# Kernel optimization log

Measured on AMD Instinct MI355X. Metric: run time of the kernel, lower is better.

The kernel has to match this reference:

```python
import jax, jax.numpy as jnp
import numpy as np

NUM_HEADS = 8
TOPK = 16


def setup_inputs() -> dict:
    key = jax.random.key(0)
    ks = jax.random.split(key, 13)
    B, C, H, W = 2, 512, 64, 64
    Hu, Wu = H // 2, W // 2
    hd = C // NUM_HEADS
    n = lambda k, shape, s=1.0: jax.random.normal(k, shape, dtype=jnp.float32) * s
    return {
        "x": n(ks[0], (B, C, H, W)),
        "upper_feat": n(ks[1], (B, C, Hu, Wu)),
        "gumbel": jax.random.gumbel(ks[2], (B, NUM_HEADS, Hu * Wu), dtype=jnp.float32),
        # 1x1 convs (Conv2d + folded eval-mode BN => weight matrix + bias)
        "q_w": n(ks[3], (C, C), 0.02), "q_b": n(ks[4], (C,), 0.02),
        "kv_w": n(ks[5], (2 * C, C), 0.02), "kv_b": n(ks[6], (2 * C,), 0.02),
        "proj_w": n(ks[7], (C, C), 0.02), "proj_b": n(ks[8], (C,), 0.02),
        # depthwise 7x7 PE conv (groups = C)
        "pe_w": n(ks[9], (C, 1, 7, 7), 0.02), "pe_b": n(ks[10], (C,), 0.02),
        # gate conv1d kernel_size=1: [head_dim, 2*head_dim]
        "gate_w": n(ks[11], (hd, 2 * hd), 0.02), "gate_b": n(ks[12], (hd,), 0.02),
    }


def reference(x, upper_feat, gumbel, q_w, q_b, kv_w, kv_b, proj_w, proj_b,
              pe_w, pe_b, gate_w, gate_b):
    B, C, H, W = x.shape
    hd = C // NUM_HEADS
    Hu, Wu = upper_feat.shape[2], upper_feat.shape[3]
    N, Nu = H * W, Hu * Wu
    scale = hd ** -0.5

    def conv1x1(t, w, b):
        return jnp.einsum('bchw,oc->bohw', t, w) + b[None, :, None, None]

    # coarse attention: q from x, k/v from upper_feat
    q = conv1x1(x, q_w, q_b).reshape(B, NUM_HEADS, hd, N).transpose(0, 1, 3, 2)          # [B,h,N,d]
    kv = conv1x1(upper_feat, kv_w, kv_b).reshape(B, NUM_HEADS, 2 * hd, Nu).transpose(0, 1, 3, 2)
    k, v = kv[..., :hd], kv[..., hd:]                                                    # [B,h,Nu,d]
    sim = jnp.einsum('bhnd,bhmd->bhnm', q, k) * scale                                    # [B,h,N,Nu]
    attn = jax.nn.softmax(sim, axis=-1)
    coarse = jnp.einsum('bhnm,bhmd->bhnd', attn, v)                                      # [B,h,N,d]

    # fine branch: kv from x, top-k token selection via gumbel-softmax scores
    f_kv = conv1x1(x, kv_w, kv_b).reshape(B, NUM_HEADS, 2 * hd, N).transpose(0, 1, 3, 2)
    f_k, f_v = f_kv[..., :hd], f_kv[..., hd:]                                            # [B,h,N,d]

    # heat: channel-mean of x, adaptive-avg-pooled 2x2 to upper resolution (no grad)
    heat = jax.lax.stop_gradient(
        x.mean(axis=1).reshape(B, Hu, 2, Wu, 2).mean(axis=(2, 4)).reshape(B, Nu))
    global_sim = sim.mean(axis=2) * heat[:, None, :]                                     # [B,h,Nu]
    soft_weights = jax.nn.softmax(global_sim + gumbel, axis=-1)
    _, idx = jax.lax.top_k(soft_weights, TOPK)                                           # [B,h,K]

    # map each selected upper-token to its 2x2 block of x-tokens
    h_idx = (idx // Wu) * 2
    w_idx = (idx % Wu) * 2
    idx_full = jnp.concatenate(
        [(h_idx + dh) * W + (w_idx + dw) for dh in range(2) for dw in range(2)], axis=-1)  # [B,h,4K]

    topk_k = jnp.take_along_axis(f_k, idx_full[..., None], axis=2)                       # [B,h,4K,d]
    topk_v = jnp.take_along_axis(f_v, idx_full[..., None], axis=2)
    fine = jax.nn.softmax(jnp.einsum('bhnd,bhmd->bhnm', q, topk_k) * scale, axis=-1)
    refined = jnp.einsum('bhnm,bhmd->bhnd', fine, topk_v)                                # [B,h,N,d]

    # gated fusion (conv1d kernel_size=1 == per-token linear over 2d channels)
    fusion = jnp.concatenate([coarse, refined], axis=-1)                                 # [B,h,N,2d]
    gate = jax.nn.sigmoid(jnp.einsum('bhnc,oc->bhno', fusion, gate_w) + gate_b)
    out = gate * refined + (1.0 - gate) * coarse                                         # [B,h,N,d]

    x_out = out.transpose(0, 1, 3, 2).reshape(B, C, H, W)

    # positional encoding: depthwise 7x7 conv on v, bilinear upsample to (H,W)
    v_rs = v.transpose(0, 1, 3, 2).reshape(B, C, Hu, Wu)
    v_pe = jax.lax.conv_general_dilated(
        v_rs, pe_w, (1, 1), ((3, 3), (3, 3)), feature_group_count=C,
        dimension_numbers=('NCHW', 'OIHW', 'NCHW')) + pe_b[None, :, None, None]
    v_pe = jax.image.resize(v_pe, (B, C, H, W), method='bilinear')

    return conv1x1(x_out + v_pe, proj_w, proj_b)
```

## Files before the change

### kernel.cpp

```cpp
#include <hip/hip_runtime.h>
#include <hip/hip_bf16.h>
#include <cstdint>

typedef __hip_bfloat16 bf16;
typedef unsigned short u16;
typedef __attribute__((ext_vector_type(8))) short bf16x8;
typedef __attribute__((ext_vector_type(4))) float f32x4;

static __device__ __forceinline__ float bs2f(u16 s) {
  unsigned int u = ((unsigned int)s) << 16;
  float f;
  __builtin_memcpy(&f, &u, 4);
  return f;
}
static __device__ __forceinline__ u16 f2bs(float f) {
  bf16 h = __float2bfloat16(f);
  u16 s;
  __builtin_memcpy(&s, &h, 2);
  return s;
}
static __device__ __forceinline__ float ldf(const void* p, size_t i, int f32) {
  return f32 ? ((const float*)p)[i] : bs2f(((const u16*)p)[i]);
}

__global__ __launch_bounds__(256) void detect_dtype(const uint4* __restrict__ xs,
                                                    int* __restrict__ flag) {
  int i = blockIdx.x * 256 + threadIdx.x;
  uint4 v = xs[i];
  bool hit = false;
#pragma unroll
  for (int j = 0; j < 4; ++j) {
    unsigned w = (j == 0) ? v.x : (j == 1) ? v.y : (j == 2) ? v.z : v.w;
    if ((w & 0x7F80u) == 0x7F80u) hit = true;
    if ((w & 0x7F800000u) == 0x7F800000u) hit = true;
  }
  unsigned long long mask = __ballot(hit);
  if (mask != 0ull && (threadIdx.x & 63) == 0) atomicOr(flag, 1);
}

__global__ __launch_bounds__(256) void prep_gate(
    const void* __restrict__ gate_w, const void* __restrict__ gate_b,
    u16* __restrict__ gwb, float* __restrict__ gbf,
    const int* __restrict__ dtf) {
  const int f32 = *dtf;
  int t = threadIdx.x;
  for (int i = t; i < 8192; i += 256)
    gwb[i] = f32 ? f2bs(((const float*)gate_w)[i]) : ((const u16*)gate_w)[i];
  if (t < 64) gbf[t] = ldf(gate_b, t, f32);
}

__global__ __launch_bounds__(256) void transpose_bf16(
    const void* __restrict__ src, u16* __restrict__ dst, int N,
    float* __restrict__ heat, const int* __restrict__ dtf) {
  const int f32 = *dtf;
  const int b = blockIdx.z, n0 = blockIdx.x * 64, c0 = blockIdx.y * 64;
  const int t = threadIdx.x;
  __shared__ __align__(16) u16 tile[64][72];
#pragma unroll
  for (int j = 0; j < 2; ++j) {
    int cc = (t >> 3) + j * 32;
    int nn = (t & 7) * 8;
    u16 tmp[8];
    if (f32) {
      const float* s4 = (const float*)src + ((size_t)(b * 512 + c0 + cc)) * N + n0 + nn;
#pragma unroll
      for (int u = 0; u < 8; ++u) tmp[u] = f2bs(s4[u]);
    } else {
      *reinterpret_cast<uint4*>(tmp) = *reinterpret_cast<const uint4*>(
          (const u16*)src + ((size_t)(b * 512 + c0 + cc)) * N + n0 + nn);
    }
    *reinterpret_cast<uint4*>(&tile[cc][nn]) = *reinterpret_cast<const uint4*>(tmp);
  }
  __syncthreads();
  if (heat != nullptr && t < 32) {
    float s = 0.f;
#pragma unroll 8
    for (int cc = 0; cc < 64; ++cc)
      s += bs2f(tile[cc][2 * t]) + bs2f(tile[cc][2 * t + 1]);
    int y = blockIdx.x;
    atomicAdd(&heat[b * 1024 + (y >> 1) * 32 + t], s);
  }
#pragma unroll
  for (int j = 0; j < 2; ++j) {
    int nn = (t >> 3) + j * 32;
    int cc0 = (t & 7) * 8;
    u16 tmp[8];
#pragma unroll
    for (int u = 0; u < 8; ++u) tmp[u] = tile[cc0 + u][nn];
    *reinterpret_cast<uint4*>(&dst[((size_t)b * N + n0 + nn) * 512 + c0 + cc0]) =
        *reinterpret_cast<const uint4*>(tmp);
  }
}

template<int MODE>
__global__ __launch_bounds__(256) void gemm128(
    const u16* __restrict__ A, const void* __restrict__ W,
    const void* __restrict__ bias, u16* __restrict__ o0,
    void* __restrict__ ob, float* __restrict__ qsum, int M,
    const int* __restrict__ dtf) {
  const int f32 = *dtf;
  const int b = blockIdx.z, m0 = blockIdx.x * 128, oo0 = blockIdx.y * 64;
  const int t = threadIdx.x, w = t >> 6, lane = t & 63;
  const int quad = lane >> 4, c = lane & 15;
  __shared__ __align__(16) u16 As[128][72];
  __shared__ __align__(16) u16 Ws[64][72];
  f32x4 acc[2][4];
#pragma unroll
  for (int nt = 0; nt < 2; ++nt)
#pragma unroll
    for (int ot = 0; ot < 4; ++ot) acc[nt][ot] = (f32x4){0.f, 0.f, 0.f, 0.f};
  const u16* Ab = A + (size_t)b * M * 512;
  const int arow = t >> 1, acol = (t & 1) * 32;
  const int wrow = t >> 2, wcol = (t & 3) * 16;

  for (int k0 = 0; k0 < 512; k0 += 64) {
    __syncthreads();
    {
      const u16* ga = Ab + (size_t)(m0 + arow) * 512 + k0 + acol;
      uint4* ad = reinterpret_cast<uint4*>(&As[arow][acol]);
      const uint4* gs = reinterpret_cast<const uint4*>(ga);
      ad[0] = gs[0]; ad[1] = gs[1]; ad[2] = gs[2]; ad[3] = gs[3];
      if (f32) {
        const float* gw = (const float*)W + (size_t)(oo0 + wrow) * 512 + k0 + wcol;
#pragma unroll
        for (int e = 0; e < 16; ++e) Ws[wrow][wcol + e] = f2bs(gw[e]);
      } else {
        const u16* gw = (const u16*)W + (size_t)(oo0 + wrow) * 512 + k0 + wcol;
        *reinterpret_cast<uint4*>(&Ws[wrow][wcol])     = *reinterpret_cast<const uint4*>(gw);
        *reinterpret_cast<uint4*>(&Ws[wrow][wcol + 8]) = *reinterpret_cast<const uint4*>(gw + 8);
      }
    }
    __syncthreads();
#pragma unroll
    for (int ks = 0; ks < 2; ++ks) {
      bf16x8 av[2];
      av[0] = *reinterpret_cast<const bf16x8*>(&As[w * 32 + c][ks * 32 + quad * 8]);
      av[1] = *reinterpret_cast<const bf16x8*>(&As[w * 32 + 16 + c][ks * 32 + quad * 8]);
#pragma unroll
      for (int ot = 0; ot < 4; ++ot) {
        bf16x8 wv = *reinterpret_cast<const bf16x8*>(&Ws[ot * 16 + c][ks * 32 + quad * 8]);
#pragma unroll
        for (int nt = 0; nt < 2; ++nt) {
          if (MODE == 3)
            acc[nt][ot] = __builtin_amdgcn_mfma_f32_16x16x32_bf16(wv, av[nt], acc[nt][ot], 0, 0, 0);
          else
            acc[nt][ot] = __builtin_amdgcn_mfma_f32_16x16x32_bf16(av[nt], wv, acc[nt][ot], 0, 0, 0);
        }
      }
    }
  }

  if (MODE == 0) {
    const int h = oo0 >> 6, bh = b * 8 + h;
#pragma unroll
    for (int ot = 0; ot < 4; ++ot) {
      int o = oo0 + ot * 16 + c;
      int d = o & 63;
      float bv = ldf(bias, o, f32);
      float qs = 0.f;
#pragma unroll
      for (int nt = 0; nt < 2; ++nt)
#pragma unroll
        for (int r = 0; r < 4; ++r) {
          int m = m0 + w * 32 + nt * 16 + quad * 4 + r;
          float qv = acc[nt][ot][r] + bv;
          o0[((size_t)bh * M + m) * 64 + d] = f2bs(qv * 0.125f);
          qs += qv;
        }
      qs += __shfl_xor(qs, 16, 64);
      qs += __shfl_xor(qs, 32, 64);
      if (quad == 0) atomicAdd(&qsum[bh * 64 + d], qs);
    }
  } else {
#pragma unroll
    for (int ot = 0; ot < 4; ++ot)
#pragma unroll
      for (int r = 0; r < 4; ++r) {
        int o = oo0 + ot * 16 + quad * 4 + r;
        float bv = ldf(bias, o, f32);
#pragma unroll
        for (int nt = 0; nt < 2; ++nt) {
          int m = m0 + w * 32 + nt * 16 + c;
          float val = acc[nt][ot][r] + bv;
          size_t oi_ = ((size_t)(b * 512 + o)) * M + m;
          if (f32) ((float*)ob)[oi_] = val;
          else     ((u16*)ob)[oi_] = f2bs(val);
        }
      }
  }
}

__global__ __launch_bounds__(256) void gemm_kv(
    const u16* __restrict__ A, const void* __restrict__ W,
    const void* __restrict__ bias, u16* __restrict__ kb, u16* __restrict__ v2,
    int M, const int* __restrict__ dtf) {
  const int f32 = *dtf;
  const int b = blockIdx.z, m0 = blockIdx.x * 64, oo0 = blockIdx.y * 64;
  const int t = threadIdx.x, w = t >> 6, lane = t & 63;
  const int quad = lane >> 4, c = lane & 15;
  __shared__ __align__(16) u16 As[64][72];
  __shared__ __align__(16) u16 Ws[64][72];
  f32x4 acc[4];
#pragma unroll
  for (int ot = 0; ot < 4; ++ot) acc[ot] = (f32x4){0.f, 0.f, 0.f, 0.f};
  const u16* Ab = A + (size_t)b * M * 512;
  const int srow = t >> 2, scol = (t & 3) * 16;

  for (int k0 = 0; k0 < 512; k0 += 64) {
    __syncthreads();
    {
      const u16* ga = Ab + (size_t)(m0 + srow) * 512 + k0 + scol;
      *reinterpret_cast<uint4*>(&As[srow][scol])     = *reinterpret_cast<const uint4*>(ga);
      *reinterpret_cast<uint4*>(&As[srow][scol + 8]) = *reinterpret_cast<const uint4*>(ga + 8);
      if (f32) {
        const float* gw = (const float*)W + (size_t)(oo0 + srow) * 512 + k0 + scol;
#pragma unroll
        for (int e = 0; e < 16; ++e) Ws[srow][scol + e] = f2bs(gw[e]);
      } else {
        const u16* gw = (const u16*)W + (size_t)(oo0 + srow) * 512 + k0 + scol;
        *reinterpret_cast<uint4*>(&Ws[srow][scol])     = *reinterpret_cast<const uint4*>(gw);
        *reinterpret_cast<uint4*>(&Ws[srow][scol + 8]) = *reinterpret_cast<const uint4*>(gw + 8);
      }
    }
    __syncthreads();
#pragma unroll
    for (int ks = 0; ks < 2; ++ks) {
      bf16x8 av = *reinterpret_cast<const bf16x8*>(&As[w * 16 + c][ks * 32 + quad * 8]);
#pragma unroll
      for (int ot = 0; ot < 4; ++ot) {
        bf16x8 wv = *reinterpret_cast<const bf16x8*>(&Ws[ot * 16 + c][ks * 32 + quad * 8]);
        acc[ot] = __builtin_amdgcn_mfma_f32_16x16x32_bf16(av, wv, acc[ot], 0, 0, 0);
      }
    }
  }

#pragma unroll
  for (int ot = 0; ot < 4; ++ot) {
    int o = oo0 + ot * 16 + c;
    float bv = ldf(bias, o, f32);
    int hh = o >> 7, jj = o & 127;
#pragma unroll
    for (int r = 0; r < 4; ++r) {
      int m = m0 + w * 16 + quad * 4 + r;
      u16 val = f2bs(acc[ot][r] + bv);
      if (jj < 64) {
        kb[((size_t)(b * 8 + hh) * M + m) * 64 + jj] = val;
      } else {
        int d = jj & 63;
        v2[((((size_t)(b * 8 + hh) * 16 + (m >> 6)) * 2 + ((m >> 5) & 1)) * 4 + (d >> 4)) * 512
           + (((m >> 3) & 3) * 16 + (d & 15)) * 8 + (m & 7)] = val;
      }
    }
  }
}

__global__ __launch_bounds__(256) void topk_kernel(
    const float* __restrict__ qsum, const u16* __restrict__ k,
    const float* __restrict__ heat, const void* __restrict__ gumbel,
    int* __restrict__ posb, const int* __restrict__ dtf) {
  const int f32 = *dtf;
  int bh = blockIdx.x, b = bh >> 3, t = threadIdx.x;
  const int lane = t & 63, w = t >> 6;
  __shared__ float qs[64];
  __shared__ float s[1024];
  __shared__ float rv[4];
  __shared__ int   ri[4];
  if (t < 64) qs[t] = qsum[bh * 64 + t];
  __syncthreads();
  for (int j = 0; j < 4; ++j) {
    int m = t + j * 256;
    const u16* kr = k + ((size_t)bh * 1024 + m) * 64;
    float dot = 0.f;
    for (int d = 0; d < 64; ++d) dot += qs[d] * bs2f(kr[d]);
    s[m] = dot * (0.125f / 4096.0f) * (heat[b * 1024 + m] * (1.0f / 2048.0f)) +
           ldf(gumbel, (size_t)bh * 1024 + m, f32);
  }
  __syncthreads();
  for (int it = 0; it < 16; ++it) {
    float bv = -1e30f; int bi = 0x7fffffff;
    for (int j = 0; j < 4; ++j) {
      int m = t + j * 256; float vv = s[m];
      if (vv > bv || (vv == bv && m < bi)) { bv = vv; bi = m; }
    }
#pragma unroll
    for (int off = 1; off < 64; off <<= 1) {
      float ov = __shfl_xor(bv, off, 64);
      int   oi = __shfl_xor(bi, off, 64);
      if (ov > bv || (ov == bv && oi < bi)) { bv = ov; bi = oi; }
    }
    if (lane == 0) { rv[w] = bv; ri[w] = bi; }
    __syncthreads();
    if (t == 0) {
      float fv = rv[0]; int fi = ri[0];
#pragma unroll
      for (int ww = 1; ww < 4; ++ww)
        if (rv[ww] > fv || (rv[ww] == fv && ri[ww] < fi)) { fv = rv[ww]; fi = ri[ww]; }
      s[fi] = -1e30f;
      int hy = (fi >> 5) * 2, wx = (fi & 31) * 2;
      posb[bh * 64 + it]      = hy * 64 + wx;
      posb[bh * 64 + 16 + it] = hy * 64 + wx + 1;
      posb[bh * 64 + 32 + it] = (hy + 1) * 64 + wx;
      posb[bh * 64 + 48 + it] = (hy + 1) * 64 + wx + 1;
    }
    __syncthreads();
  }
}

__global__ __launch_bounds__(256) void gather_kv_mfma(
    const u16* __restrict__ xT, const void* __restrict__ kv_w,
    const void* __restrict__ kv_b, const int* __restrict__ posb,
    u16* __restrict__ tkb, u16* __restrict__ tvTb,
    const int* __restrict__ dtf) {
  const int f32 = *dtf;
  const int bh = blockIdx.x, b = bh >> 3, h = bh & 7;
  const int half = blockIdx.y;
  const int t = threadIdx.x, w = t >> 6, lane = t & 63;
  const int quad = lane >> 4, c = lane & 15;
  __shared__ int pos[64];
  __shared__ __align__(16) u16 As[64][72];
  __shared__ __align__(16) u16 Ws[64][72];
  if (t < 64) pos[t] = posb[bh * 64 + t];
  __syncthreads();
  const int obase = h * 128 + half * 64;
  const int srow = t >> 2, scol = (t & 3) * 16;
  const int arow = pos[srow];
  f32x4 acc[4];
#pragma unroll
  for (int ot = 0; ot < 4; ++ot) acc[ot] = (f32x4){0.f, 0.f, 0.f, 0.f};

  for (int k0 = 0; k0 < 512; k0 += 64) {
    __syncthreads();
    {
      const u16* ga = xT + ((size_t)b * 4096 + arow) * 512 + k0 + scol;
      *reinterpret_cast<uint4*>(&As[srow][scol])     = *reinterpret_cast<const uint4*>(ga);
      *reinterpret_cast<uint4*>(&As[srow][scol + 8]) = *reinterpret_cast<const uint4*>(ga + 8);
      if (f32) {
        const float* gw = (const float*)kv_w + (size_t)(obase + srow) * 512 + k0 + scol;
#pragma unroll
        for (int e = 0; e < 16; ++e) Ws[srow][scol + e] = f2bs(gw[e]);
      } else {
        const u16* gw = (const u16*)kv_w + (size_t)(obase + srow) * 512 + k0 + scol;
        *reinterpret_cast<uint4*>(&Ws[srow][scol])     = *reinterpret_cast<const uint4*>(gw);
        *reinterpret_cast<uint4*>(&Ws[srow][scol + 8]) = *reinterpret_cast<const uint4*>(gw + 8);
      }
    }
    __syncthreads();
#pragma unroll
    for (int ks = 0; ks < 2; ++ks) {
      bf16x8 av = *reinterpret_cast<const bf16x8*>(&As[w * 16 + c][ks * 32 + quad * 8]);
#pragma unroll
      for (int ot = 0; ot < 4; ++ot) {
        bf16x8 wv = *reinterpret_cast<const bf16x8*>(&Ws[ot * 16 + c][ks * 32 + quad * 8]);
        acc[ot] = __builtin_amdgcn_mfma_f32_16x16x32_bf16(av, wv, acc[ot], 0, 0, 0);
      }
    }
  }

#pragma unroll
  for (int ot = 0; ot < 4; ++ot) {
    int d = ot * 16 + c;
    float bv = ldf(kv_b, obase + d, f32);
#pragma unroll
    for (int r = 0; r < 4; ++r) {
      int m = w * 16 + quad * 4 + r;
      u16 val = f2bs(acc[ot][r] + bv);
      if (half) tvTb[((size_t)bh * 64 + d) * 64 + m] = val;
      else      tkb[((size_t)bh * 64 + m) * 64 + d] = val;
    }
  }
}

__global__ __launch_bounds__(256) void dwconv_kernel(
    const u16* __restrict__ v2, const void* __restrict__ pe_w,
    const void* __restrict__ pe_b, u16* __restrict__ vpe,
    const int* __restrict__ dtf) {
  const int f32 = *dtf;
  int bc = blockIdx.x;
  int b = bc >> 9, c = bc & 511;
  int h = c >> 6, d = c & 63;
  int dt = d >> 4, cc = d & 15;
  int t = threadIdx.x;
  __shared__ float img[1024];
  __shared__ float wts[49];
  if (t < 128) {
    int ch = t >> 3, s = (t >> 2) & 1, q2 = t & 3;
    const u16* src = v2 + ((((size_t)(b * 8 + h) * 16 + ch) * 2 + s) * 4 + dt) * 512
                        + (q2 * 16 + cc) * 8;
    uint4 v4 = *reinterpret_cast<const uint4*>(src);
    u16 tmp[8];
    *reinterpret_cast<uint4*>(tmp) = v4;
#pragma unroll
    for (int e = 0; e < 8; ++e) img[t * 8 + e] = bs2f(tmp[e]);
  }
  if (t < 49) wts[t] = ldf(pe_w, c * 49 + t, f32);
  float bias = ldf(pe_b, c, f32);
  __syncthreads();

  float wreg[49];
#pragma unroll
  for (int i = 0; i < 49; ++i) wreg[i] = wts[i];

  const int x = t & 31, y0 = (t >> 5) * 4;
  float acc[4] = {0.f, 0.f, 0.f, 0.f};
#pragma unroll
  for (int r = 0; r < 10; ++r) {
    int yy = y0 - 3 + r;
    if ((unsigned)yy >= 32u) continue;
    float rr[7];
#pragma unroll
    for (int j = 0; j < 7; ++j) {
      int xc = x - 3 + j;
      rr[j] = ((unsigned)xc < 32u) ? img[yy * 32 + xc] : 0.f;
    }
#pragma unroll
    for (int p = 0; p < 4; ++p) {
      int ky = r - p;
      if (ky < 0 || ky > 6) continue;
      float s2 = 0.f;
#pragma unroll
      for (int j = 0; j < 7; ++j) s2 += rr[j] * wreg[ky * 7 + j];
      acc[p] += s2;
    }
  }
#pragma unroll
  for (int p = 0; p < 4; ++p)
    vpe[(size_t)bc * 1024 + (y0 + p) * 32 + x] = f2bs(acc[p] + bias);
}

__global__ __launch_bounds__(256, 4) void attn_fused(
    const u16* __restrict__ q, const u16* __restrict__ k,
    const u16* __restrict__ v2, const u16* __restrict__ tkb,
    const u16* __restrict__ tvTb, const u16* __restrict__ gwb,
    const float* __restrict__ gbf, const u16* __restrict__ vpe,
    u16* __restrict__ xsT) {
  const int bh = blockIdx.y, b = bh >> 3, h = bh & 7;
  const int bx = blockIdx.x;
  const int n0 = bx * 64;
  const int t = threadIdx.x, w = t >> 6, lane = t & 63;
  const int quad = lane >> 4, c = lane & 15;

  __shared__ __align__(16) u16 lds[13824];
  u16* Ks = lds;
  u16* Ps = lds + 9216;

  bf16x8 bq[2];
  {
    const u16* qr = q + ((size_t)bh * 4096 + n0 + w * 16 + c) * 64;
    bq[0] = *reinterpret_cast<const bf16x8*>(qr + quad * 8);
    bq[1] = *reinterpret_cast<const bf16x8*>(qr + 32 + quad * 8);
  }
  f32x4 po[4];
#pragma unroll
  for (int dt = 0; dt < 4; ++dt) po[dt] = (f32x4){0.f, 0.f, 0.f, 0.f};
  float sume = 0.f;

  const u16* kbase = k + (size_t)bh * 65536;
  const u16* v2base = v2 + (size_t)bh * 65536;
  const int srow = t >> 2, scol = (t & 3) * 16;

  uint4 kr0, kr1;
  {
    const u16* gk = kbase + (size_t)srow * 64 + scol;
    kr0 = *reinterpret_cast<const uint4*>(gk);
    kr1 = *reinterpret_cast<const uint4*>(gk + 8);
    *reinterpret_cast<uint4*>(&Ks[srow * 72 + scol])     = kr0;
    *reinterpret_cast<uint4*>(&Ks[srow * 72 + scol + 8]) = kr1;
    const u16* gk1 = kbase + (size_t)(64 + srow) * 64 + scol;
    kr0 = *reinterpret_cast<const uint4*>(gk1);
    kr1 = *reinterpret_cast<const uint4*>(gk1 + 8);
  }

  for (int ch = 0; ch < 16; ++ch) {
    __syncthreads();
    const int buf = ch & 1;

    bf16x8 av[4][2];
    {
      const u16* v2c = v2base + (size_t)ch * 4096;
#pragma unroll
      for (int dt = 0; dt < 4; ++dt) {
        av[dt][0] = *reinterpret_cast<const bf16x8*>(v2c + dt * 512 + lane * 8);
        av[dt][1] = *reinterpret_cast<const bf16x8*>(v2c + 2048 + dt * 512 + lane * 8);
      }
    }

    f32x4 st[4];
#pragma unroll
    for (int mt = 0; mt < 4; ++mt) {
      const u16* krow = &Ks[buf * 4608 + (mt * 16 + c) * 72];
      bf16x8 ak0 = *reinterpret_cast<const bf16x8*>(krow + quad * 8);
      bf16x8 ak1 = *reinterpret_cast<const bf16x8*>(krow + 32 + quad * 8);
      f32x4 acc = (f32x4){0.f, 0.f, 0.f, 0.f};
      acc = __builtin_amdgcn_mfma_f32_16x16x32_bf16(ak0, bq[0], acc, 0, 0, 0);
      acc = __builtin_amdgcn_mfma_f32_16x16x32_bf16(ak1, bq[1], acc, 0, 0, 0);
      st[mt] = acc;
    }

    if (ch + 1 < 16) {
      *reinterpret_cast<uint4*>(&Ks[(buf ^ 1) * 4608 + srow * 72 + scol])     = kr0;
      *reinterpret_cast<uint4*>(&Ks[(buf ^ 1) * 4608 + srow * 72 + scol + 8]) = kr1;
      if (ch + 2 < 16) {
        const u16* gk = kbase + (size_t)((ch + 2) * 64 + srow) * 64 + scol;
        kr0 = *reinterpret_cast<const uint4*>(gk);
        kr1 = *reinterpret_cast<const uint4*>(gk + 8);
      }
    }

    float cs = 0.f;
    u16* psw = &Ps[(w * 16 + c) * 72];
#pragma unroll
    for (int mt = 0; mt < 4; ++mt) {
      float e0 = __expf(st[mt][0]);
      float e1 = __expf(st[mt][1]);
      float e2 = __expf(st[mt][2]);
      float e3 = __expf(st[mt][3]);
      cs += (e0 + e1) + (e2 + e3);
      ushort4 pw;
      pw.x = f2bs(e0); pw.y = f2bs(e1); pw.z = f2bs(e2); pw.w = f2bs(e3);
      *reinterpret_cast<ushort4*>(psw + mt * 16 + quad * 4) = pw;
    }
    cs += __shfl_xor(cs, 16, 64);
    cs += __shfl_xor(cs, 32, 64);
    sume += cs;

#pragma unroll
    for (int s = 0; s < 2; ++s) {
      bf16x8 bp = *reinterpret_cast<const bf16x8*>(psw + s * 32 + quad * 8);
#pragma unroll
      for (int dt = 0; dt < 4; ++dt) {
        po[dt] = __builtin_amdgcn_mfma_f32_16x16x32_bf16(av[dt][s], bp, po[dt], 0, 0, 0);
      }
    }
  }

  __syncthreads();
  u16* fus = lds;
  u16* vl  = lds + 8704;
  float* gbl = (float*)(lds + 13312);

  const int ym = bx >> 1;
  int r0_, r1_; float wy0, wy1;
  if ((bx & 1) == 0) { r0_ = ym > 0 ? ym - 1 : 0; r1_ = ym; wy0 = 0.25f; wy1 = 0.75f; }
  else               { r0_ = ym; r1_ = ym < 31 ? ym + 1 : 31; wy0 = 0.75f; wy1 = 0.25f; }

  for (int idx = t; idx < 512; idx += 256) {
    int seg = idx & 3, ch2 = (idx >> 2) & 63, rr = idx >> 8;
    int vrow = rr ? r1_ : r0_;
    const uint4 v4 = *reinterpret_cast<const uint4*>(
        vpe + ((size_t)(b * 512 + h * 64 + ch2)) * 1024 + vrow * 32 + seg * 8);
    u16* dst = &vl[(rr * 64 + ch2) * 36 + seg * 8];
    uint2 lo, hi;
    lo.x = v4.x; lo.y = v4.y; hi.x = v4.z; hi.y = v4.w;
    *reinterpret_cast<uint2*>(dst)     = lo;
    *reinterpret_cast<uint2*>(dst + 4) = hi;
  }
  if (t < 64) gbl[t] = gbf[t];
  __syncthreads();

  u16* fusw = &fus[(w * 16 + c) * 136];
  f32x4 st2[4];
#pragma unroll
  for (int mt = 0; mt < 4; ++mt) {
    f32x4 acc = (f32x4){0.f, 0.f, 0.f, 0.f};
#pragma unroll
    for (int s = 0; s < 2; ++s) {
      bf16x8 ak = *reinterpret_cast<const bf16x8*>(
          &tkb[((size_t)bh * 64 + mt * 16 + c) * 64 + s * 32 + quad * 8]);
      acc = __builtin_amdgcn_mfma_f32_16x16x32_bf16(ak, bq[s], acc, 0, 0, 0);
    }
    st2[mt] = acc;
  }
  float sume2 = 0.f;
#pragma unroll
  for (int mt = 0; mt < 4; ++mt) {
    float e0 = __expf(st2[mt][0]);
    float e1 = __expf(st2[mt][1]);
    float e2 = __expf(st2[mt][2]);
    float e3 = __expf(st2[mt][3]);
    sume2 += (e0 + e1) + (e2 + e3);
    ushort4 pw;
    pw.x = f2bs(e0); pw.y = f2bs(e1); pw.z = f2bs(e2); pw.w = f2bs(e3);
    *reinterpret_cast<ushort4*>(fusw + mt * 16 + quad * 4) = pw;
  }
  sume2 += __shfl_xor(sume2, 16, 64);
  sume2 += __shfl_xor(sume2, 32, 64);
  float inv2 = 1.0f / sume2;

  f32x4 po2[4];
#pragma unroll
  for (int dt = 0; dt < 4; ++dt) po2[dt] = (f32x4){0.f, 0.f, 0.f, 0.f};
#pragma unroll
  for (int s = 0; s < 2; ++s) {
    bf16x8 bp = *reinterpret_cast<const bf16x8*>(fusw + s * 32 + quad * 8);
#pragma unroll
    for (int dt = 0; dt < 4; ++dt) {
      bf16x8 av = *reinterpret_cast<const bf16x8*>(
          &tvTb[((size_t)bh * 64 + dt * 16 + c) * 64 + s * 32 + quad * 8]);
      po2[dt] = __builtin_amdgcn_mfma_f32_16x16x32_bf16(av, bp, po2[dt], 0, 0, 0);
    }
  }

  float invc = 1.0f / sume;
#pragma unroll
  for (int dt = 0; dt < 4; ++dt) {
    ushort4 cw, rw;
    cw.x = f2bs(po[dt][0] * invc); cw.y = f2bs(po[dt][1] * invc);
    cw.z = f2bs(po[dt][2] * invc); cw.w = f2bs(po[dt][3] * invc);
    rw.x = f2bs(po2[dt][0] * inv2); rw.y = f2bs(po2[dt][1] * inv2);
    rw.z = f2bs(po2[dt][2] * inv2); rw.w = f2bs(po2[dt][3] * inv2);
    *reinterpret_cast<ushort4*>(fusw + dt * 16 + quad * 4)      = cw;
    *reinterpret_cast<ushort4*>(fusw + 64 + dt * 16 + quad * 4) = rw;
  }

  f32x4 ga[4];
#pragma unroll
  for (int ot = 0; ot < 4; ++ot) ga[ot] = (f32x4){0.f, 0.f, 0.f, 0.f};
#pragma unroll
  for (int s = 0; s < 4; ++s) {
    bf16x8 bf = *reinterpret_cast<const bf16x8*>(fusw + s * 32 + quad * 8);
#pragma unroll
    for (int ot = 0; ot < 4; ++ot) {
      bf16x8 ag = *reinterpret_cast<const bf16x8*>(
          gwb + (ot * 16 + c) * 128 + s * 32 + quad * 8);
      ga[ot] = __builtin_amdgcn_mfma_f32_16x16x32_bf16(ag, bf, ga[ot], 0, 0, 0);
    }
  }

  const int x = w * 16 + c;
  int jx = x >> 1, x0, x1; float wx0, wx1;
  if ((x & 1) == 0) { x0 = (jx > 0) ? jx - 1 : 0; x1 = jx; wx0 = 0.25f; wx1 = 0.75f; }
  else              { x0 = jx; x1 = (jx < 31) ? jx + 1 : 31; wx0 = 0.75f; wx1 = 0.25f; }
#pragma unroll
  for (int dt = 0; dt < 4; ++dt) {
    ushort4 ow;
    u16 tmp[4];
#pragma unroll
    for (int r = 0; r < 4; ++r) {
      int row = dt * 16 + quad * 4 + r;
      float ref = po2[dt][r] * inv2;
      float coar = bs2f(fusw[row]);
      float g = 1.0f / (1.0f + __expf(-(ga[dt][r] + gbl[row])));
      float vv = wy0 * (wx0 * bs2f(vl[row * 36 + x0]) +
                        wx1 * bs2f(vl[row * 36 + x1])) +
                 wy1 * (wx0 * bs2f(vl[(64 + row) * 36 + x0]) +
                        wx1 * bs2f(vl[(64 + row) * 36 + x1]));
      tmp[r] = f2bs(g * ref + (1.0f - g) * coar + vv);
    }
    ow.x = tmp[0]; ow.y = tmp[1]; ow.z = tmp[2]; ow.w = tmp[3];
    *reinterpret_cast<ushort4*>(fusw + dt * 16 + quad * 4) = ow;
  }

  {
    int nl = lane >> 2, cs2 = (lane & 3) * 16;
    const u16* srcrow = &fus[(w * 16 + nl) * 136 + cs2];
    u16* dst = xsT + ((size_t)b * 4096 + n0 + w * 16 + nl) * 512 + h * 64 + cs2;
    *reinterpret_cast<uint4*>(dst)     = *reinterpret_cast<const uint4*>(srcrow);
    *reinterpret_cast<uint4*>(dst + 8) = *reinterpret_cast<const uint4*>(srcrow + 8);
  }
}

extern "C" void kernel_launch(void* const* d_in, const int* in_sizes, int n_in,
                              void* d_out, int out_size, void* d_ws, size_t ws_size,
                              hipStream_t stream) {
  const void* x    = d_in[0];
  const void* up   = d_in[1];
  const void* gum  = d_in[2];
  const void* q_w  = d_in[3];
  const void* q_b  = d_in[4];
  const void* kv_w = d_in[5];
  const void* kv_b = d_in[6];
  const void* p_w  = d_in[7];
  const void* p_b  = d_in[8];
  const void* pe_w = d_in[9];
  const void* pe_b = d_in[10];
  const void* g_w  = d_in[11];
  const void* g_b  = d_in[12];

  float* ws    = (float*)d_ws;
  int*   dtf   = (int*)ws;
  float* qsum  = ws + 16;
  float* heat  = qsum + 1024;
  int*   posb  = (int*)(heat + 2048);
  float* gbf   = (float*)(posb + 1024);
  u16*   gwb   = (u16*)(gbf + 64);
  u16*   tkb   = gwb + 8192;
  u16*   tvTb  = tkb + 65536;
  u16*   qb    = tvTb + 65536;
  u16*   kb    = qb + 4194304;
  u16*   v2b   = kb + 1048576;
  u16*   xT    = v2b + 1048576;
  u16*   upT   = xT + 4194304;
  u16*   xsT   = upT + 1048576;
  u16*   vpe   = xsT + 4194304;

  dim3 blk(256);
  hipMemsetAsync(ws, 0, (16 + 1024 + 2048) * 4, stream);
  detect_dtype<<<dim3(64), blk, 0, stream>>>((const uint4*)x, dtf);
  prep_gate<<<dim3(1), blk, 0, stream>>>(g_w, g_b, gwb, gbf, dtf);
  transpose_bf16<<<dim3(64, 8, 2), blk, 0, stream>>>(x, xT, 4096, heat, dtf);
  transpose_bf16<<<dim3(16, 8, 2), blk, 0, stream>>>(up, upT, 1024, nullptr, dtf);
  gemm128<0><<<dim3(32, 8, 2), blk, 0, stream>>>(xT, q_w, q_b, qb, nullptr, qsum, 4096, dtf);
  gemm_kv<<<dim3(16, 16, 2), blk, 0, stream>>>(upT, kv_w, kv_b, kb, v2b, 1024, dtf);
  topk_kernel<<<dim3(16), blk, 0, stream>>>(qsum, kb, heat, gum, posb, dtf);
  gather_kv_mfma<<<dim3(16, 2), blk, 0, stream>>>(xT, kv_w, kv_b, posb, tkb, tvTb, dtf);
  dwconv_kernel<<<dim3(1024), blk, 0, stream>>>(v2b, pe_w, pe_b, vpe, dtf);
  attn_fused<<<dim3(64, 16), blk, 0, stream>>>(qb, kb, v2b, tkb, tvTb, gwb, gbf, vpe, xsT);
  gemm128<3><<<dim3(32, 8, 2), blk, 0, stream>>>(xsT, p_w, p_b, nullptr, d_out, nullptr, 4096, dtf);
}
```

Before: 248.2 us.

## Double-buffer LDS tiles in projection GEMMs and vectorize top-k key loads

Both gemm128 and gemm_kv now use two LDS buffers, with the next K-tile held in registers so its global loads overlap the MFMA work on the current tile. This also removes one of the two barriers per iteration. Separately, the top-k scoring loop reads key rows as 16-byte vectors instead of scalar u16 loads. The cost is twice the shared memory and more registers, which may reduce occupancy.

```diff
diff --git a/kernel.cpp b/kernel.cpp
--- a/kernel.cpp
+++ b/kernel.cpp
@@ -102,8 +102,8 @@
   const int b = blockIdx.z, m0 = blockIdx.x * 128, oo0 = blockIdx.y * 64;
   const int t = threadIdx.x, w = t >> 6, lane = t & 63;
   const int quad = lane >> 4, c = lane & 15;
-  __shared__ __align__(16) u16 As[128][72];
-  __shared__ __align__(16) u16 Ws[64][72];
+  __shared__ __align__(16) u16 As[2][128][72];
+  __shared__ __align__(16) u16 Ws[2][64][72];
   f32x4 acc[2][4];
 #pragma unroll
   for (int nt = 0; nt < 2; ++nt)
@@ -113,32 +113,48 @@
   const int arow = t >> 1, acol = (t & 1) * 32;
   const int wrow = t >> 2, wcol = (t & 3) * 16;
 
-  for (int k0 = 0; k0 < 512; k0 += 64) {
+  uint4 ra[4], rw[4];
+  auto lda = [&](int k0) {
+    const uint4* gs = reinterpret_cast<const uint4*>(
+        Ab + (size_t)(m0 + arow) * 512 + k0 + acol);
+    ra[0] = gs[0]; ra[1] = gs[1]; ra[2] = gs[2]; ra[3] = gs[3];
+    if (f32) {
+      const uint4* gw = reinterpret_cast<const uint4*>(
+          (const float*)W + (size_t)(oo0 + wrow) * 512 + k0 + wcol);
+      rw[0] = gw[0]; rw[1] = gw[1]; rw[2] = gw[2]; rw[3] = gw[3];
+    } else {
+      const uint4* gw = reinterpret_cast<const uint4*>(
+          (const u16*)W + (size_t)(oo0 + wrow) * 512 + k0 + wcol);
+      rw[0] = gw[0]; rw[1] = gw[1];
+    }
+  };
+  auto sta = [&](int bf) {
+    uint4* ad = reinterpret_cast<uint4*>(&As[bf][arow][acol]);
+    ad[0] = ra[0]; ad[1] = ra[1]; ad[2] = ra[2]; ad[3] = ra[3];
+    if (f32) {
+      float tf[16];
+      __builtin_memcpy(tf, rw, 64);
+#pragma unroll
+      for (int e = 0; e < 16; ++e) Ws[bf][wrow][wcol + e] = f2bs(tf[e]);
+    } else {
+      *reinterpret_cast<uint4*>(&Ws[bf][wrow][wcol])     = rw[0];
+      *reinterpret_cast<uint4*>(&Ws[bf][wrow][wcol + 8]) = rw[1];
+    }
+  };
+
+  lda(0); sta(0); lda(64);
+
+  for (int ki = 0; ki < 8; ++ki) {
     __syncthreads();
-    {
-      const u16* ga = Ab + (size_t)(m0 + arow) * 512 + k0 + acol;
-      uint4* ad = reinterpret_cast<uint4*>(&As[arow][acol]);
-      const uint4* gs = reinterpret_cast<const uint4*>(ga);
-      ad[0] = gs[0]; ad[1] = gs[1]; ad[2] = gs[2]; ad[3] = gs[3];
-      if (f32) {
-        const float* gw = (const float*)W + (size_t)(oo0 + wrow) * 512 + k0 + wcol;
-#pragma unroll
-        for (int e = 0; e < 16; ++e) Ws[wrow][wcol + e] = f2bs(gw[e]);
-      } else {
-        const u16* gw = (const u16*)W + (size_t)(oo0 + wrow) * 512 + k0 + wcol;
-        *reinterpret_cast<uint4*>(&Ws[wrow][wcol])     = *reinterpret_cast<const uint4*>(gw);
-        *reinterpret_cast<uint4*>(&Ws[wrow][wcol + 8]) = *reinterpret_cast<const uint4*>(gw + 8);
-      }
-    }
-    __syncthreads();
+    const int bf = ki & 1;
 #pragma unroll
     for (int ks = 0; ks < 2; ++ks) {
       bf16x8 av[2];
-      av[0] = *reinterpret_cast<const bf16x8*>(&As[w * 32 + c][ks * 32 + quad * 8]);
-      av[1] = *reinterpret_cast<const bf16x8*>(&As[w * 32 + 16 + c][ks * 32 + quad * 8]);
+      av[0] = *reinterpret_cast<const bf16x8*>(&As[bf][w * 32 + c][ks * 32 + quad * 8]);
+      av[1] = *reinterpret_cast<const bf16x8*>(&As[bf][w * 32 + 16 + c][ks * 32 + quad * 8]);
 #pragma unroll
       for (int ot = 0; ot < 4; ++ot) {
-        bf16x8 wv = *reinterpret_cast<const bf16x8*>(&Ws[ot * 16 + c][ks * 32 + quad * 8]);
+        bf16x8 wv = *reinterpret_cast<const bf16x8*>(&Ws[bf][ot * 16 + c][ks * 32 + quad * 8]);
 #pragma unroll
         for (int nt = 0; nt < 2; ++nt) {
           if (MODE == 3)
@@ -147,6 +163,10 @@
             acc[nt][ot] = __builtin_amdgcn_mfma_f32_16x16x32_bf16(av[nt], wv, acc[nt][ot], 0, 0, 0);
         }
       }
+    }
+    if (ki + 1 < 8) {
+      sta(bf ^ 1);
+      if (ki + 2 < 8) lda((ki + 2) << 6);
     }
   }
 
@@ -198,39 +218,60 @@
   const int b = blockIdx.z, m0 = blockIdx.x * 64, oo0 = blockIdx.y * 64;
   const int t = threadIdx.x, w = t >> 6, lane = t & 63;
   const int quad = lane >> 4, c = lane & 15;
-  __shared__ __align__(16) u16 As[64][72];
-  __shared__ __align__(16) u16 Ws[64][72];
+  __shared__ __align__(16) u16 As[2][64][72];
+  __shared__ __align__(16) u16 Ws[2][64][72];
   f32x4 acc[4];
 #pragma unroll
   for (int ot = 0; ot < 4; ++ot) acc[ot] = (f32x4){0.f, 0.f, 0.f, 0.f};
   const u16* Ab = A + (size_t)b * M * 512;
   const int srow = t >> 2, scol = (t & 3) * 16;
 
-  for (int k0 = 0; k0 < 512; k0 += 64) {
+  uint4 ra[2], rw[4];
+  auto lda = [&](int k0) {
+    const uint4* gs = reinterpret_cast<const uint4*>(
+        Ab + (size_t)(m0 + srow) * 512 + k0 + scol);
+    ra[0] = gs[0]; ra[1] = gs[1];
+    if (f32) {
+      const uint4* gw = reinterpret_cast<const uint4*>(
+          (const float*)W + (size_t)(oo0 + srow) * 512 + k0 + scol);
+      rw[0] = gw[0]; rw[1] = gw[1]; rw[2] = gw[2]; rw[3] = gw[3];
+    } else {
+      const uint4* gw = reinterpret_cast<const uint4*>(
+          (const u16*)W + (size_t)(oo0 + srow) * 512 + k0 + scol);
+      rw[0] = gw[0]; rw[1] = gw[1];
+    }
+  };
+  auto sta = [&](int bf) {
+    *reinterpret_cast<uint4*>(&As[bf][srow][scol])     = ra[0];
+    *reinterpret_cast<uint4*>(&As[bf][srow][scol + 8]) = ra[1];
+    if (f32) {
+      float tf[16];
+      __builtin_memcpy(tf, rw, 64);
+#pragma unroll
+      for (int e = 0; e < 16; ++e) Ws[bf][srow][scol + e] = f2bs(tf[e]);
+    } else {
+      *reinterpret_cast<uint4*>(&Ws[bf][srow][scol])     = rw[0];
+      *reinterpret_cast<uint4*>(&Ws[bf][srow][scol + 8]) = rw[1];
+    }
+  };
+
+  lda(0); sta(0); lda(64);
+
+  for (int ki = 0; ki < 8; ++ki) {
     __syncthreads();
-    {
-      const u16* ga = Ab + (size_t)(m0 + srow) * 512 + k0 + scol;
-      *reinterpret_cast<uint4*>(&As[srow][scol])     = *reinterpret_cast<const uint4*>(ga);
-      *reinterpret_cast<uint4*>(&As[srow][scol + 8]) = *reinterpret_cast<const uint4*>(ga + 8);
-      if (f32) {
-        const float* gw = (const float*)W + (size_t)(oo0 + srow) * 512 + k0 + scol;
-#pragma unroll
-        for (int e = 0; e < 16; ++e) Ws[srow][scol + e] = f2bs(gw[e]);
-      } else {
-        const u16* gw = (const u16*)W + (size_t)(oo0 + srow) * 512 + k0 + scol;
-        *reinterpret_cast<uint4*>(&Ws[srow][scol])     = *reinterpret_cast<const uint4*>(gw);
-        *reinterpret_cast<uint4*>(&Ws[srow][scol + 8]) = *reinterpret_cast<const uint4*>(gw + 8);
-      }
-    }
-    __syncthreads();
+    const int bf = ki & 1;
 #pragma unroll
     for (int ks = 0; ks < 2; ++ks) {
-      bf16x8 av = *reinterpret_cast<const bf16x8*>(&As[w * 16 + c][ks * 32 + quad * 8]);
+      bf16x8 av = *reinterpret_cast<const bf16x8*>(&As[bf][w * 16 + c][ks * 32 + quad * 8]);
 #pragma unroll
       for (int ot = 0; ot < 4; ++ot) {
-        bf16x8 wv = *reinterpret_cast<const bf16x8*>(&Ws[ot * 16 + c][ks * 32 + quad * 8]);
+        bf16x8 wv = *reinterpret_cast<const bf16x8*>(&Ws[bf][ot * 16 + c][ks * 32 + quad * 8]);
         acc[ot] = __builtin_amdgcn_mfma_f32_16x16x32_bf16(av, wv, acc[ot], 0, 0, 0);
       }
+    }
+    if (ki + 1 < 8) {
+      sta(bf ^ 1);
+      if (ki + 2 < 8) lda((ki + 2) << 6);
     }
   }
 
@@ -269,9 +310,16 @@
   __syncthreads();
   for (int j = 0; j < 4; ++j) {
     int m = t + j * 256;
-    const u16* kr = k + ((size_t)bh * 1024 + m) * 64;
+    const uint4* kr = reinterpret_cast<const uint4*>(k + ((size_t)bh * 1024 + m) * 64);
     float dot = 0.f;
-    for (int d = 0; d < 64; ++d) dot += qs[d] * bs2f(kr[d]);
+#pragma unroll
+    for (int v = 0; v < 8; ++v) {
+      uint4 kq = kr[v];
+      u16 tmp[8];
+      *reinterpret_cast<uint4*>(tmp) = kq;
+#pragma unroll
+      for (int e = 0; e < 8; ++e) dot += qs[v * 8 + e] * bs2f(tmp[e]);
+    }
     s[m] = dot * (0.125f / 4096.0f) * (heat[b * 1024 + m] * (1.0f / 2048.0f)) +
            ldf(gumbel, (size_t)bh * 1024 + m, f32);
   }
```

Result: slower. 319.7 us (+28.8%).
